# Optimization experiments

Measured on AMD Instinct MI355X. Metric: run time of the kernel, lower is better.

Reference implementation:

```python
import jax, jax.numpy as jnp
import numpy as np

D_MODEL = 1024
N_HEADS = 16
D_FF = 4096
B = 8
S_TGT = 1024
S_SRC = 1024


def layer_norm(x, g, b, eps=1e-5):
    mu = jnp.mean(x, axis=-1, keepdims=True)
    var = jnp.mean(jnp.square(x - mu), axis=-1, keepdims=True)
    return (x - mu) * jax.lax.rsqrt(var + eps) * g + b


def mha(q_in, k_in, v_in, Wq, bq, Wk, bk, Wv, bv, Wo, bo, mask):
    Bq, Sq, D = q_in.shape
    hd = D // N_HEADS

    def split(t):
        return t.reshape(t.shape[0], t.shape[1], N_HEADS, hd).transpose(0, 2, 1, 3)

    Q = split(q_in @ Wq + bq)   # [B,H,Sq,hd]
    K = split(k_in @ Wk + bk)   # [B,H,Sk,hd]
    V = split(v_in @ Wv + bv)
    scores = jnp.einsum('bhqd,bhkd->bhqk', Q, K) / jnp.sqrt(jnp.float32(hd))
    scores = jnp.where(mask, scores, jnp.float32(-1e9))
    attn = jax.nn.softmax(scores, axis=-1)
    out = jnp.einsum('bhqk,bhkd->bhqd', attn, V)
    out = out.transpose(0, 2, 1, 3).reshape(Bq, Sq, D)
    return out @ Wo + bo


def setup_inputs() -> dict:
    key = jax.random.key(0)
    ks = jax.random.split(key, 32)
    s = 0.02
    inp = {
        'x': jax.random.normal(ks[0], (B, S_TGT, D_MODEL), dtype=jnp.float32),
        'encoder_output': jax.random.normal(ks[1], (B, S_SRC, D_MODEL), dtype=jnp.float32),
        'tgt_mask': jnp.tril(jnp.ones((S_TGT, S_TGT), dtype=bool))[None, None],
        'src_mask': jnp.ones((1, 1, S_TGT, S_SRC), dtype=bool),
    }
    i = 2
    for p in ('sa', 'ca'):
        for w in ('Wq', 'Wk', 'Wv', 'Wo'):
            inp[f'{p}_{w}'] = jax.random.normal(ks[i], (D_MODEL, D_MODEL), dtype=jnp.float32) * s
            inp[f'{p}_b{w[1].lower()}'] = jnp.zeros((D_MODEL,), dtype=jnp.float32)
            i += 1
    inp['ff_W1'] = jax.random.normal(ks[i], (D_MODEL, D_FF), dtype=jnp.float32) * s; i += 1
    inp['ff_b1'] = jnp.zeros((D_FF,), dtype=jnp.float32)
    inp['ff_W2'] = jax.random.normal(ks[i], (D_FF, D_MODEL), dtype=jnp.float32) * s; i += 1
    inp['ff_b2'] = jnp.zeros((D_MODEL,), dtype=jnp.float32)
    for n in ('ln1', 'ln2', 'ln3'):
        inp[f'{n}_g'] = jnp.ones((D_MODEL,), dtype=jnp.float32)
        inp[f'{n}_b'] = jnp.zeros((D_MODEL,), dtype=jnp.float32)
    return inp


def reference(x, encoder_output, tgt_mask, src_mask,
              sa_Wq, sa_bq, sa_Wk, sa_bk, sa_Wv, sa_bv, sa_Wo, sa_bo,
              ca_Wq, ca_bq, ca_Wk, ca_bk, ca_Wv, ca_bv, ca_Wo, ca_bo,
              ff_W1, ff_b1, ff_W2, ff_b2,
              ln1_g, ln1_b, ln2_g, ln2_b, ln3_g, ln3_b):
    # masked self-attention + residual + LN (dropout = identity in eval mode)
    attn = mha(x, x, x, sa_Wq, sa_bq, sa_Wk, sa_bk, sa_Wv, sa_bv, sa_Wo, sa_bo, tgt_mask)
    x = layer_norm(x + attn, ln1_g, ln1_b)
    # cross-attention to encoder output
    cross = mha(x, encoder_output, encoder_output,
                ca_Wq, ca_bq, ca_Wk, ca_bk, ca_Wv, ca_bv, ca_Wo, ca_bo, src_mask)
    x = layer_norm(x + cross, ln2_g, ln2_b)
    # position-wise FFN: Linear -> ReLU -> Linear
    ff = jax.nn.relu(x @ ff_W1 + ff_b1) @ ff_W2 + ff_b2
    x = layer_norm(x + ff, ln3_g, ln3_b)
    return x
```

## Files before the change

kernel.cpp:

```cpp
#include <hip/hip_runtime.h>
#include <math.h>

typedef __attribute__((ext_vector_type(8))) short short8;
typedef __attribute__((ext_vector_type(4))) short short4v;
typedef __attribute__((ext_vector_type(4))) float floatx4;

__device__ inline float bf2f(unsigned short h) {
    unsigned int u = ((unsigned int)h) << 16;
    float f;
    __builtin_memcpy(&f, &u, 4);
    return f;
}
__device__ inline unsigned short f2bf(float f) {
    unsigned int u;
    __builtin_memcpy(&u, &f, 4);
    u = (u + 0x7fffu + ((u >> 16) & 1u)) >> 16;
    return (unsigned short)u;
}
__device__ inline unsigned int f2u(float f) {
    return __builtin_bit_cast(unsigned int, f);
}

__device__ inline void gld_lds16(const unsigned short* g, unsigned short* l) {
    __builtin_amdgcn_global_load_lds(
        (const __attribute__((address_space(1))) unsigned int*)g,
        (__attribute__((address_space(3))) unsigned int*)l, 16, 0, 0);
}

__global__ __launch_bounds__(256) void detect_dtype(
    const unsigned short* __restrict__ x, int* __restrict__ flag) {
    __shared__ int s[4];
    int bad = 0;
    for (int i = threadIdx.x; i < 8192; i += 256) {
        float v = bf2f(x[i]);
        if (!(fabsf(v) <= 1.0e4f)) bad = 1;
    }
    unsigned long long b = __ballot(bad);
    int wave = threadIdx.x >> 6;
    if ((threadIdx.x & 63) == 0) s[wave] = (b != 0ULL) ? 1 : 0;
    __syncthreads();
    if (threadIdx.x == 0) flag[0] = s[0] | s[1] | s[2] | s[3];
}

__global__ __launch_bounds__(256) void to_bf16_kernel(
    const void* __restrict__ in, unsigned short* __restrict__ out,
    const int* __restrict__ flag, int n8) {
    int fl = flag[0];
    int i = blockIdx.x * 256 + threadIdx.x;
    if (i >= n8) return;
    size_t off = (size_t)i * 8;
    if (fl) {
        floatx4 f0 = *(const floatx4*)((const float*)in + off);
        floatx4 f1 = *(const floatx4*)((const float*)in + off + 4);
        short8 v;
#pragma unroll
        for (int j = 0; j < 4; j++) {
            v[j] = (short)f2bf(f0[j]);
            v[4 + j] = (short)f2bf(f1[j]);
        }
        *(short8*)(out + off) = v;
    } else {
        *(short8*)(out + off) = *(const short8*)((const unsigned short*)in + off);
    }
}

__global__ __launch_bounds__(256) void transpose_any(
    const void* __restrict__ in, unsigned short* __restrict__ out,
    int rows, int cols, const int* __restrict__ flag) {
    int fl = flag ? flag[0] : 0;
    __shared__ unsigned short t[32][33];
    int tx = threadIdx.x & 31, ty = threadIdx.x >> 5;
    int c0 = blockIdx.x * 32, r0 = blockIdx.y * 32;
    size_t base = (size_t)blockIdx.z * rows * cols;
#pragma unroll
    for (int k = 0; k < 4; k++) {
        size_t idx = base + (size_t)(r0 + ty + k * 8) * cols + c0 + tx;
        t[ty + k * 8][tx] = fl ? f2bf(((const float*)in)[idx])
                               : ((const unsigned short*)in)[idx];
    }
    __syncthreads();
#pragma unroll
    for (int k = 0; k < 4; k++)
        out[base + (size_t)(c0 + ty + k * 8) * rows + r0 + tx] = t[tx][ty + k * 8];
}

struct Ptr8 { const void* p[8]; };
__global__ __launch_bounds__(256) void transpose8(
    Ptr8 in, unsigned short* __restrict__ out, const int* __restrict__ flag) {
    int fl = flag[0];
    __shared__ unsigned short t[32][33];
    const void* src = in.p[blockIdx.z];
    unsigned short* dst = out + (size_t)blockIdx.z * 1024 * 1024;
    int tx = threadIdx.x & 31, ty = threadIdx.x >> 5;
    int c0 = blockIdx.x * 32, r0 = blockIdx.y * 32;
#pragma unroll
    for (int k = 0; k < 4; k++) {
        size_t idx = (size_t)(r0 + ty + k * 8) * 1024 + c0 + tx;
        t[ty + k * 8][tx] = fl ? f2bf(((const float*)src)[idx])
                               : ((const unsigned short*)src)[idx];
    }
    __syncthreads();
#pragma unroll
    for (int k = 0; k < 4; k++)
        dst[(size_t)(c0 + ty + k * 8) * 1024 + r0 + tx] = t[tx][ty + k * 8];
}

__device__ inline void stage_half(const unsigned short* __restrict__ G, int ldk,
                                  int grow, int gcol, unsigned short* ldsb,
                                  int tid) {
    int s0 = tid, s1 = tid + 512;
    int r0 = s0 >> 3, c0 = ((s0 & 7) ^ (r0 & 7)) << 3;
    int r1 = s1 >> 3, c1 = ((s1 & 7) ^ (r1 & 7)) << 3;
    gld_lds16(&G[(size_t)(grow + r0) * ldk + gcol + c0], &ldsb[s0 * 8]);
    gld_lds16(&G[(size_t)(grow + r1) * ldk + gcol + c1], &ldsb[s1 * 8]);
}

template <int BN_, int EPI>
__global__ __launch_bounds__(512) void gemm8(
    const unsigned short* __restrict__ A, const unsigned short* __restrict__ Bt,
    const void* __restrict__ b0, const void* __restrict__ b1,
    const void* __restrict__ b2, unsigned short* __restrict__ C0,
    unsigned short* __restrict__ C1, unsigned short* __restrict__ C2,
    int M, int N, int K, const int* __restrict__ flag) {
    constexpr int NR = BN_ / 64;
    constexpr int WNT = BN_ / 4;
    constexpr int ASZ = 16384;
    constexpr int BSZ = BN_ * 64;
    __shared__ alignas(16) unsigned short lds[2 * ASZ + 2 * BSZ];

    const int tid = threadIdx.x;
    const int lane = tid & 63, wave = tid >> 6;
    const int quad = lane >> 4, l16 = lane & 15, x7 = l16 & 7;
    const int wm = wave >> 2, wn = wave & 3;
    const int bm = blockIdx.x * 256, bn = blockIdx.y * BN_;
    const int NT = K >> 6;

    floatx4 acc[8][NR];
#pragma unroll
    for (int i = 0; i < 8; ++i)
#pragma unroll
        for (int j = 0; j < NR; ++j) acc[i][j] = (floatx4){0.f, 0.f, 0.f, 0.f};

    stage_half(A, K, bm, 0, lds, tid);
    stage_half(A, K, bm + 128, 0, lds + 8192, tid);
    stage_half(Bt, K, bn, 0, lds + 2 * ASZ, tid);
    if (BN_ == 256) stage_half(Bt, K, bn + 128, 0, lds + 2 * ASZ + 8192, tid);
    asm volatile("s_waitcnt vmcnt(0)" ::: "memory");
    __builtin_amdgcn_s_barrier();

    short8 bfr[NR][2], afr[2][2][2];

    for (int it = 0; it < NT; ++it) {
        unsigned short* const Ac = lds + (it & 1) * ASZ;
        unsigned short* const Bc = lds + 2 * ASZ + (it & 1) * BSZ;
        unsigned short* const An = lds + ((it + 1) & 1) * ASZ;
        unsigned short* const Bn = lds + 2 * ASZ + ((it + 1) & 1) * BSZ;
        const bool more = (it + 1 < NT);
        if (more) {
            const int kn = (it + 1) << 6;
            stage_half(A, K, bm, kn, An, tid);
            stage_half(A, K, bm + 128, kn, An + 8192, tid);
            stage_half(Bt, K, bn, kn, Bn, tid);
            if (BN_ == 256) stage_half(Bt, K, bn + 128, kn, Bn + 8192, tid);
        }
#pragma unroll
        for (int ni = 0; ni < NR; ++ni)
#pragma unroll
            for (int ks = 0; ks < 2; ++ks)
                bfr[ni][ks] = *(const short8*)&Bc[
                    (wn * WNT + ni * 16 + l16) * 64 +
                    ((((ks << 2) + quad) ^ x7) << 3)];
#pragma unroll
        for (int m2 = 0; m2 < 2; ++m2)
#pragma unroll
            for (int ks = 0; ks < 2; ++ks)
                afr[0][m2][ks] = *(const short8*)&Ac[
                    (wm * 128 + m2 * 16 + l16) * 64 +
                    ((((ks << 2) + quad) ^ x7) << 3)];
#pragma unroll
        for (int q = 0; q < 4; ++q) {
            if (q < 3) {
#pragma unroll
                for (int m2 = 0; m2 < 2; ++m2)
#pragma unroll
                    for (int ks = 0; ks < 2; ++ks)
                        afr[(q + 1) & 1][m2][ks] = *(const short8*)&Ac[
                            (wm * 128 + ((q + 1) * 2 + m2) * 16 + l16) * 64 +
                            ((((ks << 2) + quad) ^ x7) << 3)];
            }
            __builtin_amdgcn_s_setprio(1);
#pragma unroll
            for (int m2 = 0; m2 < 2; ++m2)
#pragma unroll
                for (int ni = 0; ni < NR; ++ni) {
                    acc[q * 2 + m2][ni] = __builtin_amdgcn_mfma_f32_16x16x32_bf16(
                        bfr[ni][0], afr[q & 1][m2][0], acc[q * 2 + m2][ni], 0, 0, 0);
                    acc[q * 2 + m2][ni] = __builtin_amdgcn_mfma_f32_16x16x32_bf16(
                        bfr[ni][1], afr[q & 1][m2][1], acc[q * 2 + m2][ni], 0, 0, 0);
                }
            __builtin_amdgcn_s_setprio(0);
        }
        if (more) {
            asm volatile("s_waitcnt vmcnt(0)" ::: "memory");
            __builtin_amdgcn_s_barrier();
        }
    }

    const int fl = flag[0];
    const void* bp = b0;
    unsigned short* Cp = C0;
    int mode = 0;
    int cb = bn;
    if (EPI == 1) mode = 1;
    if (EPI == 4) mode = 2;
    if (EPI == 2) {
        int ch = bn >> 10;
        cb = bn & 1023;
        bp = (ch == 0) ? b0 : (ch == 1) ? b1 : b2;
        Cp = (ch == 0) ? C0 : (ch == 1) ? C1 : C2;
        mode = (ch == 0) ? 2 : (ch == 1) ? 3 : 4;
    }
    if (EPI == 3) {
        int ch = bn >> 10;
        cb = bn & 1023;
        bp = (ch == 0) ? b0 : b1;
        Cp = (ch == 0) ? C0 : C1;
        mode = (ch == 0) ? 3 : 4;
    }
#pragma unroll
    for (int ni = 0; ni < NR; ++ni) {
        const int colb = cb + wn * WNT + ni * 16 + quad * 4;
        float b4[4];
        if (fl) {
            floatx4 t = *(const floatx4*)&((const float*)bp)[colb];
#pragma unroll
            for (int r = 0; r < 4; ++r) b4[r] = t[r];
        } else {
            short4v t = *(const short4v*)&((const unsigned short*)bp)[colb];
#pragma unroll
            for (int r = 0; r < 4; ++r) b4[r] = bf2f((unsigned short)t[r]);
        }
        const int hh = colb >> 6, dd = colb & 63;
#pragma unroll
        for (int mi = 0; mi < 8; ++mi) {
            const int row = bm + wm * 128 + mi * 16 + l16;
            short4v pk;
#pragma unroll
            for (int r = 0; r < 4; ++r) {
                float v = acc[mi][ni][r] + b4[r];
                if (mode == 1) v = fmaxf(v, 0.f);
                if (mode == 2) v *= 0.18033688f;
                pk[r] = (short)f2bf(v);
            }
            if (mode <= 1) {
                *(short4v*)&Cp[(size_t)row * N + colb] = pk;
            } else {
                const int b_ = row >> 10, s_ = row & 1023;
                if (mode != 4) {
                    *(short4v*)&Cp[((((size_t)b_ * 16 + hh) * 1024) + s_) * 64 + dd] = pk;
                } else {
#pragma unroll
                    for (int r = 0; r < 4; ++r)
                        Cp[(((size_t)b_ * 16 + hh) * 64 + dd + r) * 1024 + s_] =
                            (unsigned short)pk[r];
                }
            }
        }
    }
}

template <int CAUSAL>
__global__ __launch_bounds__(256) void attn_kernel(
    const unsigned short* __restrict__ Q, const unsigned short* __restrict__ K,
    const unsigned short* __restrict__ Vt, unsigned short* __restrict__ O,
    int Skv) {
    __shared__ alignas(16) unsigned short Ks[512 * 8];
    __shared__ alignas(16) unsigned short Vs[512 * 8];
    const int S = 1024;
    int tid = threadIdx.x, wave = tid >> 6, lane = tid & 63;
    int quad = lane >> 4, l16 = lane & 15;
    int fid = blockIdx.y * 8 + blockIdx.x;
    int bh = fid & 127;
    int qt = fid >> 7;
    if (CAUSAL) qt = 7 - qt;
    int qbA = qt * 128 + wave * 32;
    int qbB = qbA + 16;
    const unsigned short* Qp = Q + (size_t)bh * S * 64;
    const unsigned short* Kp = K + (size_t)bh * Skv * 64;
    const unsigned short* Vp = Vt + (size_t)bh * 64 * Skv;

    short8 qA0 = *(const short8*)&Qp[(qbA + l16) * 64 + quad * 8];
    short8 qA1 = *(const short8*)&Qp[(qbA + l16) * 64 + 32 + quad * 8];
    short8 qB0 = *(const short8*)&Qp[(qbB + l16) * 64 + quad * 8];
    short8 qB1 = *(const short8*)&Qp[(qbB + l16) * 64 + 32 + quad * 8];

    floatx4 oA[4], oB[4];
#pragma unroll
    for (int ni = 0; ni < 4; ni++) {
        oA[ni] = (floatx4){0.f, 0.f, 0.f, 0.f};
        oB[ni] = (floatx4){0.f, 0.f, 0.f, 0.f};
    }
    float mA = -1e30f, lA = 0.f, mB = -1e30f, lB = 0.f;
    int kend = CAUSAL ? (qt + 1) * 128 : Skv;

    int sr0 = tid >> 3, sc0 = (tid & 7) ^ (sr0 & 7);
    int sr1 = (tid + 256) >> 3, sc1 = ((tid + 256) & 7) ^ (sr1 & 7);
    int shA = l16 + (((2 * quad) & 3) << 4);
    int shB = l16 + (((2 * quad + 1) & 3) << 4);

    for (int kb = 0; kb < kend; kb += 64) {
        gld_lds16(&Kp[(size_t)(kb + sr0) * 64 + sc0 * 8], &Ks[tid * 8]);
        gld_lds16(&Kp[(size_t)(kb + sr1) * 64 + sc1 * 8], &Ks[(tid + 256) * 8]);
        gld_lds16(&Vp[(size_t)sr0 * Skv + kb + sc0 * 8], &Vs[tid * 8]);
        gld_lds16(&Vp[(size_t)sr1 * Skv + kb + sc1 * 8], &Vs[(tid + 256) * 8]);
        __syncthreads();

        auto tile = [&](const short8& q0, const short8& q1, floatx4(&o)[4],
                        float& m, float& l, int qb) {
            if (CAUSAL && kb > qb + 15) return;
            floatx4 st[4];
#pragma unroll
            for (int c = 0; c < 4; c++) {
                int row = c * 16 + l16, r7 = row & 7;
                short8 kf0 = *(const short8*)&Ks[(row * 8 + (quad ^ r7)) * 8];
                short8 kf1 = *(const short8*)&Ks[(row * 8 + ((quad + 4) ^ r7)) * 8];
                floatx4 z = (floatx4){0.f, 0.f, 0.f, 0.f};
                z = __builtin_amdgcn_mfma_f32_16x16x32_bf16(kf0, q0, z, 0, 0, 0);
                z = __builtin_amdgcn_mfma_f32_16x16x32_bf16(kf1, q1, z, 0, 0, 0);
                st[c] = z;
            }
            if (CAUSAL && (kb + 63 > qb)) {
#pragma unroll
                for (int c = 0; c < 4; c++)
#pragma unroll
                    for (int r = 0; r < 4; r++) {
                        int kk = kb + c * 16 + quad * 4 + r;
                        if (kk > qb + l16) st[c][r] = -1e30f;
                    }
            }
            float t0 = fmaxf(fmaxf(st[0][0], st[0][1]), st[0][2]);
            float t1 = fmaxf(fmaxf(st[0][3], st[1][0]), st[1][1]);
            float t2 = fmaxf(fmaxf(st[1][2], st[1][3]), st[2][0]);
            float t3 = fmaxf(fmaxf(st[2][1], st[2][2]), st[2][3]);
            float t4 = fmaxf(fmaxf(st[3][0], st[3][1]), st[3][2]);
            float smax = fmaxf(fmaxf(fmaxf(t0, t1), fmaxf(t2, t3)),
                               fmaxf(t4, st[3][3]));
            smax = fmaxf(smax, __shfl_xor(smax, 16));
            smax = fmaxf(smax, __shfl_xor(smax, 32));
            float mi = m;
            if (!__all(smax <= m + 8.f)) {
                mi = fmaxf(m, smax);
                float alpha = exp2f(m - mi);
                l *= alpha;
#pragma unroll
                for (int ni = 0; ni < 4; ni++) o[ni] *= alpha;
                m = mi;
            }
            float rs = 0.f;
#pragma unroll
            for (int c = 0; c < 4; c++)
#pragma unroll
                for (int r = 0; r < 4; r++) {
                    float p = exp2f(st[c][r] - mi);
                    st[c][r] = p;
                    rs += p;
                }
            rs += __shfl_xor(rs, 16);
            rs += __shfl_xor(rs, 32);
            l += rs;

            unsigned int pd[4][2];
#pragma unroll
            for (int c = 0; c < 4; c++) {
                pd[c][0] = __builtin_amdgcn_perm(f2u(st[c][1]), f2u(st[c][0]),
                                                 0x07060302u);
                pd[c][1] = __builtin_amdgcn_perm(f2u(st[c][3]), f2u(st[c][2]),
                                                 0x07060302u);
            }
            short8 pf[2];
#pragma unroll
            for (int h = 0; h < 2; h++) {
                unsigned int a0 = __shfl((int)pd[2 * h][0], shA);
                unsigned int a1 = __shfl((int)pd[2 * h][1], shA);
                unsigned int a2 = __shfl((int)pd[2 * h][0], shB);
                unsigned int a3 = __shfl((int)pd[2 * h][1], shB);
                unsigned int b0 = __shfl((int)pd[2 * h + 1][0], shA);
                unsigned int b1 = __shfl((int)pd[2 * h + 1][1], shA);
                unsigned int b2 = __shfl((int)pd[2 * h + 1][0], shB);
                unsigned int b3 = __shfl((int)pd[2 * h + 1][1], shB);
                unsigned int dw[4];
                dw[0] = (quad < 2) ? a0 : b0;
                dw[1] = (quad < 2) ? a1 : b1;
                dw[2] = (quad < 2) ? a2 : b2;
                dw[3] = (quad < 2) ? a3 : b3;
                __builtin_memcpy(&pf[h], dw, 16);
            }
#pragma unroll
            for (int ni = 0; ni < 4; ni++) {
                int row = ni * 16 + l16, r7 = row & 7;
                short8 vf0 = *(const short8*)&Vs[(row * 8 + (quad ^ r7)) * 8];
                short8 vf1 = *(const short8*)&Vs[(row * 8 + ((quad + 4) ^ r7)) * 8];
                o[ni] = __builtin_amdgcn_mfma_f32_16x16x32_bf16(vf0, pf[0], o[ni], 0, 0, 0);
                o[ni] = __builtin_amdgcn_mfma_f32_16x16x32_bf16(vf1, pf[1], o[ni], 0, 0, 0);
            }
        };
        tile(qA0, qA1, oA, mA, lA, qbA);
        tile(qB0, qB1, oB, mB, lB, qbB);
        __syncthreads();
    }

    int b = bh >> 4, h = bh & 15;
    float invA = 1.0f / lA, invB = 1.0f / lB;
    size_t qrowA = ((size_t)(b * S + qbA + l16)) * 1024 + h * 64;
    size_t qrowB = ((size_t)(b * S + qbB + l16)) * 1024 + h * 64;
#pragma unroll
    for (int ni = 0; ni < 4; ni++) {
        short4v p4;
#pragma unroll
        for (int r = 0; r < 4; r++) p4[r] = (short)f2bf(oA[ni][r] * invA);
        *(short4v*)&O[qrowA + ni * 16 + quad * 4] = p4;
#pragma unroll
        for (int r = 0; r < 4; r++) p4[r] = (short)f2bf(oB[ni][r] * invB);
        *(short4v*)&O[qrowB + ni * 16 + quad * 4] = p4;
    }
}

template <int AEXT, int OEXT>
__global__ __launch_bounds__(256) void add_ln_kernel(
    const void* __restrict__ A, const unsigned short* __restrict__ Bv,
    const void* __restrict__ g, const void* __restrict__ be,
    void* __restrict__ out, const int* __restrict__ flag) {
    int fl = flag[0];
    __shared__ float red[2][4];
    int row = blockIdx.x, tid = threadIdx.x;
    size_t base = (size_t)row * 1024;
    int c = tid * 4;
    float v[4], sum = 0.f, ss = 0.f;
    if (AEXT && fl) {
        floatx4 af = *(const floatx4*)&((const float*)A)[base + c];
#pragma unroll
        for (int k = 0; k < 4; k++) v[k] = af[k];
    } else {
        short4v av = *(const short4v*)&((const unsigned short*)A)[base + c];
#pragma unroll
        for (int k = 0; k < 4; k++) v[k] = bf2f((unsigned short)av[k]);
    }
    short4v bv = *(const short4v*)&Bv[base + c];
#pragma unroll
    for (int k = 0; k < 4; k++) {
        v[k] += bf2f((unsigned short)bv[k]);
        sum += v[k];
        ss += v[k] * v[k];
    }
#pragma unroll
    for (int off = 1; off < 64; off <<= 1) {
        sum += __shfl_xor(sum, off);
        ss += __shfl_xor(ss, off);
    }
    int wave = tid >> 6, lane = tid & 63;
    if (lane == 0) {
        red[0][wave] = sum;
        red[1][wave] = ss;
    }
    __syncthreads();
    sum = red[0][0] + red[0][1] + red[0][2] + red[0][3];
    ss = red[1][0] + red[1][1] + red[1][2] + red[1][3];
    float mu = sum * (1.0f / 1024.0f);
    float var = ss * (1.0f / 1024.0f) - mu * mu;
    float rstd = rsqrtf(var + 1e-5f);
#pragma unroll
    for (int k = 0; k < 4; k++) {
        float gv = fl ? ((const float*)g)[c + k]
                      : bf2f(((const unsigned short*)g)[c + k]);
        float bev = fl ? ((const float*)be)[c + k]
                       : bf2f(((const unsigned short*)be)[c + k]);
        float y = (v[k] - mu) * rstd * gv + bev;
        if (OEXT && fl)
            ((float*)out)[base + c + k] = y;
        else
            ((unsigned short*)out)[base + c + k] = f2bf(y);
    }
}

extern "C" void kernel_launch(void* const* d_in, const int* in_sizes, int n_in,
                              void* d_out, int out_size, void* d_ws, size_t ws_size,
                              hipStream_t stream) {
    const int M = 8192;
    typedef const void* cvp;
    cvp x = d_in[0];
    cvp enc = d_in[1];
    cvp saWq = d_in[4], sabq = d_in[5];
    cvp saWk = d_in[6], sabk = d_in[7];
    cvp saWv = d_in[8], sabv = d_in[9];
    cvp saWo = d_in[10], sabo = d_in[11];
    cvp caWq = d_in[12], cabq = d_in[13];
    cvp caWk = d_in[14], cabk = d_in[15];
    cvp caWv = d_in[16], cabv = d_in[17];
    cvp caWo = d_in[18], cabo = d_in[19];
    cvp ffW1 = d_in[20], ffb1 = d_in[21];
    cvp ffW2 = d_in[22], ffb2 = d_in[23];
    cvp ln1g = d_in[24], ln1b = d_in[25];
    cvp ln2g = d_in[26], ln2b = d_in[27];
    cvp ln3g = d_in[28], ln3b = d_in[29];

    char* ws = (char*)d_ws;
    const size_t MB = 1024 * 1024;
    typedef unsigned short* up;
    up wt_sa_qkv = (up)(ws + 0);
    up wt_sa_o   = (up)(ws + 6 * MB);
    up wt_ca_q   = (up)(ws + 8 * MB);
    up wt_ca_kv  = (up)(ws + 10 * MB);
    up wt_ca_o   = (up)(ws + 14 * MB);
    up wtff1     = (up)(ws + 16 * MB);
    up wtff2     = (up)(ws + 24 * MB);
    up Qb  = (up)(ws + 32 * MB);
    up Kb  = (up)(ws + 48 * MB);
    up Vtb = (up)(ws + 64 * MB);
    up xb  = (up)(ws + 80 * MB);
    up Hb  = (up)(ws + 32 * MB);
    up Ob  = (up)(ws + 96 * MB);
    up Pb  = (up)(ws + 112 * MB);
    up x1  = (up)(ws + 128 * MB);
    up x2  = (up)(ws + 144 * MB);
    up encb = (up)(ws + 144 * MB);
    int* flag = (int*)(ws + 160 * MB);

    dim3 blk(256), blk5(512);
    detect_dtype<<<1, blk, 0, stream>>>((const unsigned short*)x, flag);

    to_bf16_kernel<<<4096, blk, 0, stream>>>(x, xb, flag, M * 1024 / 8);
    to_bf16_kernel<<<4096, blk, 0, stream>>>(enc, encb, flag, M * 1024 / 8);

    Ptr8 w8;
    w8.p[0] = saWq; w8.p[1] = saWk; w8.p[2] = saWv; w8.p[3] = saWo;
    w8.p[4] = caWq; w8.p[5] = caWk; w8.p[6] = caWv; w8.p[7] = caWo;
    transpose8<<<dim3(32, 32, 8), blk, 0, stream>>>(w8, (up)(ws + 0), flag);
    transpose_any<<<dim3(128, 32, 1), blk, 0, stream>>>(ffW1, wtff1, 1024, 4096, flag);
    transpose_any<<<dim3(32, 128, 1), blk, 0, stream>>>(ffW2, wtff2, 4096, 1024, flag);

    gemm8<256, 2><<<dim3(32, 12), blk5, 0, stream>>>(
        xb, wt_sa_qkv, sabq, sabk, sabv, Qb, Kb, Vtb, M, 3072, 1024, flag);
    attn_kernel<1><<<dim3(8, 128), blk, 0, stream>>>(Qb, Kb, Vtb, Ob, 1024);
    gemm8<128, 0><<<dim3(32, 8), blk5, 0, stream>>>(
        Ob, wt_sa_o, sabo, nullptr, nullptr, Pb, nullptr, nullptr, M, 1024, 1024, flag);
    add_ln_kernel<1, 0><<<dim3(8192), blk, 0, stream>>>(x, Pb, ln1g, ln1b, x1, flag);

    gemm8<128, 4><<<dim3(32, 8), blk5, 0, stream>>>(
        x1, wt_ca_q, cabq, nullptr, nullptr, Qb, nullptr, nullptr, M, 1024, 1024, flag);
    gemm8<256, 3><<<dim3(32, 8), blk5, 0, stream>>>(
        encb, wt_ca_kv, cabk, cabv, nullptr, Kb, Vtb, nullptr, M, 2048, 1024, flag);
    attn_kernel<0><<<dim3(8, 128), blk, 0, stream>>>(Qb, Kb, Vtb, Ob, 1024);
    gemm8<128, 0><<<dim3(32, 8), blk5, 0, stream>>>(
        Ob, wt_ca_o, cabo, nullptr, nullptr, Pb, nullptr, nullptr, M, 1024, 1024, flag);
    add_ln_kernel<0, 0><<<dim3(8192), blk, 0, stream>>>(x1, Pb, ln2g, ln2b, x2, flag);

    gemm8<256, 1><<<dim3(32, 16), blk5, 0, stream>>>(
        x2, wtff1, ffb1, nullptr, nullptr, Hb, nullptr, nullptr, M, 4096, 1024, flag);
    gemm8<128, 0><<<dim3(32, 8), blk5, 0, stream>>>(
        Hb, wtff2, ffb2, nullptr, nullptr, Pb, nullptr, nullptr, M, 1024, 4096, flag);
    add_ln_kernel<0, 1><<<dim3(8192), blk, 0, stream>>>(x2, Pb, ln3g, ln3b, d_out, flag);
}
```

Before: 774.4 us.

## Double-buffer K/V tiles in attention and merge the two query sub-tiles' work

The attention kernel gets ping-pong LDS buffers, so the next K/V chunk loads while the current one is being computed, and the trailing barrier is replaced by a waitcnt plus barrier. The QK^T and PV MFMAs for both 16-row query sub-tiles are interleaved so each K/V fragment is read from LDS once and shared between them, and s_setprio is raised around the MFMA sections. The softmax row sum now comes from an MFMA against a ones vector instead of an exp sum plus shuffles, which also rounds the row sum to bf16 precision. This doubles LDS use and may cut occupancy.

```diff
diff --git a/kernel.cpp b/kernel.cpp
--- a/kernel.cpp
+++ b/kernel.cpp
@@ -274,8 +274,8 @@
     const unsigned short* __restrict__ Q, const unsigned short* __restrict__ K,
     const unsigned short* __restrict__ Vt, unsigned short* __restrict__ O,
     int Skv) {
-    __shared__ alignas(16) unsigned short Ks[512 * 8];
-    __shared__ alignas(16) unsigned short Vs[512 * 8];
+    __shared__ alignas(16) unsigned short Ks[2][512 * 8];
+    __shared__ alignas(16) unsigned short Vs[2][512 * 8];
     const int S = 1024;
     int tid = threadIdx.x, wave = tid >> 6, lane = tid & 63;
     int quad = lane >> 4, l16 = lane & 15;
@@ -301,112 +301,157 @@
         oB[ni] = (floatx4){0.f, 0.f, 0.f, 0.f};
     }
     float mA = -1e30f, lA = 0.f, mB = -1e30f, lB = 0.f;
-    int kend = CAUSAL ? (qt + 1) * 128 : Skv;
+    const int kend = CAUSAL ? (qt + 1) * 128 : Skv;
+    const int nch = kend >> 6;
 
     int sr0 = tid >> 3, sc0 = (tid & 7) ^ (sr0 & 7);
     int sr1 = (tid + 256) >> 3, sc1 = ((tid + 256) & 7) ^ (sr1 & 7);
     int shA = l16 + (((2 * quad) & 3) << 4);
     int shB = l16 + (((2 * quad + 1) & 3) << 4);
 
-    for (int kb = 0; kb < kend; kb += 64) {
-        gld_lds16(&Kp[(size_t)(kb + sr0) * 64 + sc0 * 8], &Ks[tid * 8]);
-        gld_lds16(&Kp[(size_t)(kb + sr1) * 64 + sc1 * 8], &Ks[(tid + 256) * 8]);
-        gld_lds16(&Vp[(size_t)sr0 * Skv + kb + sc0 * 8], &Vs[tid * 8]);
-        gld_lds16(&Vp[(size_t)sr1 * Skv + kb + sc1 * 8], &Vs[(tid + 256) * 8]);
-        __syncthreads();
-
-        auto tile = [&](const short8& q0, const short8& q1, floatx4(&o)[4],
-                        float& m, float& l, int qb) {
-            if (CAUSAL && kb > qb + 15) return;
-            floatx4 st[4];
+    short8 vone;
+    {
+        unsigned int dw[4] = {0x3F803F80u, 0x3F803F80u, 0x3F803F80u, 0x3F803F80u};
+        __builtin_memcpy(&vone, dw, 16);
+    }
+
+    auto stageKV = [&](int kb, int b) {
+        gld_lds16(&Kp[(size_t)(kb + sr0) * 64 + sc0 * 8], &Ks[b][tid * 8]);
+        gld_lds16(&Kp[(size_t)(kb + sr1) * 64 + sc1 * 8], &Ks[b][(tid + 256) * 8]);
+        gld_lds16(&Vp[(size_t)sr0 * Skv + kb + sc0 * 8], &Vs[b][tid * 8]);
+        gld_lds16(&Vp[(size_t)sr1 * Skv + kb + sc1 * 8], &Vs[b][(tid + 256) * 8]);
+    };
+
+    stageKV(0, 0);
+    asm volatile("s_waitcnt vmcnt(0)" ::: "memory");
+    __builtin_amdgcn_s_barrier();
+
+    for (int ic = 0; ic < nch; ++ic) {
+        const int kb = ic << 6, cur = ic & 1;
+        const unsigned short* Ksc = Ks[cur];
+        const unsigned short* Vsc = Vs[cur];
+        if (ic + 1 < nch) stageKV(kb + 64, cur ^ 1);
+
+        const bool doA = !CAUSAL || (kb <= qbA + 15);
+        const bool doB = !CAUSAL || (kb <= qbB + 15);
+
+        if (doB) {
+            floatx4 stA[4], stB[4];
+            __builtin_amdgcn_s_setprio(1);
 #pragma unroll
             for (int c = 0; c < 4; c++) {
                 int row = c * 16 + l16, r7 = row & 7;
-                short8 kf0 = *(const short8*)&Ks[(row * 8 + (quad ^ r7)) * 8];
-                short8 kf1 = *(const short8*)&Ks[(row * 8 + ((quad + 4) ^ r7)) * 8];
-                floatx4 z = (floatx4){0.f, 0.f, 0.f, 0.f};
-                z = __builtin_amdgcn_mfma_f32_16x16x32_bf16(kf0, q0, z, 0, 0, 0);
-                z = __builtin_amdgcn_mfma_f32_16x16x32_bf16(kf1, q1, z, 0, 0, 0);
-                st[c] = z;
+                short8 kf0 = *(const short8*)&Ksc[(row * 8 + (quad ^ r7)) * 8];
+                short8 kf1 = *(const short8*)&Ksc[(row * 8 + ((quad + 4) ^ r7)) * 8];
+                if (doA) {
+                    floatx4 z = (floatx4){0.f, 0.f, 0.f, 0.f};
+                    z = __builtin_amdgcn_mfma_f32_16x16x32_bf16(kf0, qA0, z, 0, 0, 0);
+                    z = __builtin_amdgcn_mfma_f32_16x16x32_bf16(kf1, qA1, z, 0, 0, 0);
+                    stA[c] = z;
+                }
+                floatx4 y = (floatx4){0.f, 0.f, 0.f, 0.f};
+                y = __builtin_amdgcn_mfma_f32_16x16x32_bf16(kf0, qB0, y, 0, 0, 0);
+                y = __builtin_amdgcn_mfma_f32_16x16x32_bf16(kf1, qB1, y, 0, 0, 0);
+                stB[c] = y;
             }
-            if (CAUSAL && (kb + 63 > qb)) {
+            __builtin_amdgcn_s_setprio(0);
+
+            auto softmax_pack = [&](floatx4(&st)[4], float& m, float& l,
+                                    floatx4(&o)[4], short8(&pf)[2], int qb) {
+                if (CAUSAL && (kb + 63 > qb)) {
+#pragma unroll
+                    for (int c = 0; c < 4; c++)
+#pragma unroll
+                        for (int r = 0; r < 4; r++) {
+                            int kk = kb + c * 16 + quad * 4 + r;
+                            if (kk > qb + l16) st[c][r] = -1e30f;
+                        }
+                }
+                float t0 = fmaxf(fmaxf(st[0][0], st[0][1]), st[0][2]);
+                float t1 = fmaxf(fmaxf(st[0][3], st[1][0]), st[1][1]);
+                float t2 = fmaxf(fmaxf(st[1][2], st[1][3]), st[2][0]);
+                float t3 = fmaxf(fmaxf(st[2][1], st[2][2]), st[2][3]);
+                float t4 = fmaxf(fmaxf(st[3][0], st[3][1]), st[3][2]);
+                float smax = fmaxf(fmaxf(fmaxf(t0, t1), fmaxf(t2, t3)),
+                                   fmaxf(t4, st[3][3]));
+                smax = fmaxf(smax, __shfl_xor(smax, 16));
+                smax = fmaxf(smax, __shfl_xor(smax, 32));
+                float mi = m;
+                if (!__all(smax <= m + 8.f)) {
+                    mi = fmaxf(m, smax);
+                    float alpha = exp2f(m - mi);
+                    l *= alpha;
+#pragma unroll
+                    for (int ni = 0; ni < 4; ni++) o[ni] *= alpha;
+                    m = mi;
+                }
 #pragma unroll
                 for (int c = 0; c < 4; c++)
 #pragma unroll
-                    for (int r = 0; r < 4; r++) {
-                        int kk = kb + c * 16 + quad * 4 + r;
-                        if (kk > qb + l16) st[c][r] = -1e30f;
-                    }
+                    for (int r = 0; r < 4; r++) st[c][r] = exp2f(st[c][r] - mi);
+                unsigned int pd[4][2];
+#pragma unroll
+                for (int c = 0; c < 4; c++) {
+                    pd[c][0] = __builtin_amdgcn_perm(f2u(st[c][1]), f2u(st[c][0]),
+                                                     0x07060302u);
+                    pd[c][1] = __builtin_amdgcn_perm(f2u(st[c][3]), f2u(st[c][2]),
+                                                     0x07060302u);
+                }
+#pragma unroll
+                for (int h = 0; h < 2; h++) {
+                    unsigned int a0 = __shfl((int)pd[2 * h][0], shA);
+                    unsigned int a1 = __shfl((int)pd[2 * h][1], shA);
+                    unsigned int a2 = __shfl((int)pd[2 * h][0], shB);
+                    unsigned int a3 = __shfl((int)pd[2 * h][1], shB);
+                    unsigned int b0 = __shfl((int)pd[2 * h + 1][0], shA);
+                    unsigned int b1 = __shfl((int)pd[2 * h + 1][1], shA);
+                    unsigned int b2 = __shfl((int)pd[2 * h + 1][0], shB);
+                    unsigned int b3 = __shfl((int)pd[2 * h + 1][1], shB);
+                    unsigned int dw[4];
+                    dw[0] = (quad < 2) ? a0 : b0;
+                    dw[1] = (quad < 2) ? a1 : b1;
+                    dw[2] = (quad < 2) ? a2 : b2;
+                    dw[3] = (quad < 2) ? a3 : b3;
+                    __builtin_memcpy(&pf[h], dw, 16);
+                }
+            };
+
+            short8 pfA[2], pfB[2];
+            if (doA) softmax_pack(stA, mA, lA, oA, pfA, qbA);
+            softmax_pack(stB, mB, lB, oB, pfB, qbB);
+
+            __builtin_amdgcn_s_setprio(1);
+            if (doA) {
+                floatx4 zA = (floatx4){0.f, 0.f, 0.f, 0.f};
+                zA = __builtin_amdgcn_mfma_f32_16x16x32_bf16(vone, pfA[0], zA, 0, 0, 0);
+                zA = __builtin_amdgcn_mfma_f32_16x16x32_bf16(vone, pfA[1], zA, 0, 0, 0);
+                lA += zA[0];
             }
-            float t0 = fmaxf(fmaxf(st[0][0], st[0][1]), st[0][2]);
-            float t1 = fmaxf(fmaxf(st[0][3], st[1][0]), st[1][1]);
-            float t2 = fmaxf(fmaxf(st[1][2], st[1][3]), st[2][0]);
-            float t3 = fmaxf(fmaxf(st[2][1], st[2][2]), st[2][3]);
-            float t4 = fmaxf(fmaxf(st[3][0], st[3][1]), st[3][2]);
-            float smax = fmaxf(fmaxf(fmaxf(t0, t1), fmaxf(t2, t3)),
-                               fmaxf(t4, st[3][3]));
-            smax = fmaxf(smax, __shfl_xor(smax, 16));
-            smax = fmaxf(smax, __shfl_xor(smax, 32));
-            float mi = m;
-            if (!__all(smax <= m + 8.f)) {
-                mi = fmaxf(m, smax);
-                float alpha = exp2f(m - mi);
-                l *= alpha;
-#pragma unroll
-                for (int ni = 0; ni < 4; ni++) o[ni] *= alpha;
-                m = mi;
-            }
-            float rs = 0.f;
-#pragma unroll
-            for (int c = 0; c < 4; c++)
-#pragma unroll
-                for (int r = 0; r < 4; r++) {
-                    float p = exp2f(st[c][r] - mi);
-                    st[c][r] = p;
-                    rs += p;
-                }
-            rs += __shfl_xor(rs, 16);
-            rs += __shfl_xor(rs, 32);
-            l += rs;
-
-            unsigned int pd[4][2];
-#pragma unroll
-            for (int c = 0; c < 4; c++) {
-                pd[c][0] = __builtin_amdgcn_perm(f2u(st[c][1]), f2u(st[c][0]),
-                                                 0x07060302u);
-                pd[c][1] = __builtin_amdgcn_perm(f2u(st[c][3]), f2u(st[c][2]),
-                                                 0x07060302u);
-            }
-            short8 pf[2];
-#pragma unroll
-            for (int h = 0; h < 2; h++) {
-                unsigned int a0 = __shfl((int)pd[2 * h][0], shA);
-                unsigned int a1 = __shfl((int)pd[2 * h][1], shA);
-                unsigned int a2 = __shfl((int)pd[2 * h][0], shB);
-                unsigned int a3 = __shfl((int)pd[2 * h][1], shB);
-                unsigned int b0 = __shfl((int)pd[2 * h + 1][0], shA);
-                unsigned int b1 = __shfl((int)pd[2 * h + 1][1], shA);
-                unsigned int b2 = __shfl((int)pd[2 * h + 1][0], shB);
-                unsigned int b3 = __shfl((int)pd[2 * h + 1][1], shB);
-                unsigned int dw[4];
-                dw[0] = (quad < 2) ? a0 : b0;
-                dw[1] = (quad < 2) ? a1 : b1;
-                dw[2] = (quad < 2) ? a2 : b2;
-                dw[3] = (quad < 2) ? a3 : b3;
-                __builtin_memcpy(&pf[h], dw, 16);
+            {
+                floatx4 zB = (floatx4){0.f, 0.f, 0.f, 0.f};
+                zB = __builtin_amdgcn_mfma_f32_16x16x32_bf16(vone, pfB[0], zB, 0, 0, 0);
+                zB = __builtin_amdgcn_mfma_f32_16x16x32_bf16(vone, pfB[1], zB, 0, 0, 0);
+                lB += zB[0];
             }
 #pragma unroll
             for (int ni = 0; ni < 4; ni++) {
                 int row = ni * 16 + l16, r7 = row & 7;
-                short8 vf0 = *(const short8*)&Vs[(row * 8 + (quad ^ r7)) * 8];
-                short8 vf1 = *(const short8*)&Vs[(row * 8 + ((quad + 4) ^ r7)) * 8];
-                o[ni] = __builtin_amdgcn_mfma_f32_16x16x32_bf16(vf0, pf[0], o[ni], 0, 0, 0);
-                o[ni] = __builtin_amdgcn_mfma_f32_16x16x32_bf16(vf1, pf[1], o[ni], 0, 0, 0);
+                short8 vf0 = *(const short8*)&Vsc[(row * 8 + (quad ^ r7)) * 8];
+                short8 vf1 = *(const short8*)&Vsc[(row * 8 + ((quad + 4) ^ r7)) * 8];
+                if (doA) {
+                    oA[ni] = __builtin_amdgcn_mfma_f32_16x16x32_bf16(vf0, pfA[0], oA[ni], 0, 0, 0);
+                    oA[ni] = __builtin_amdgcn_mfma_f32_16x16x32_bf16(vf1, pfA[1], oA[ni], 0, 0, 0);
+                }
+                oB[ni] = __builtin_amdgcn_mfma_f32_16x16x32_bf16(vf0, pfB[0], oB[ni], 0, 0, 0);
+                oB[ni] = __builtin_amdgcn_mfma_f32_16x16x32_bf16(vf1, pfB[1], oB[ni], 0, 0, 0);
             }
-        };
-        tile(qA0, qA1, oA, mA, lA, qbA);
-        tile(qB0, qB1, oB, mB, lB, qbB);
-        __syncthreads();
+            __builtin_amdgcn_s_setprio(0);
+        }
+
+        if (ic + 1 < nch) {
+            asm volatile("s_waitcnt vmcnt(0)" ::: "memory");
+            __builtin_amdgcn_s_barrier();
+        }
     }
 
     int b = bh >> 4, h = bh & 15;
```

New measurement: 783.9 us. Within noise of the previous version (+1.2%).
